# Kernel optimization log

Measured on AMD Instinct MI355X. Metric: run time of the kernel, lower is better.

Reference implementation:

```python
import jax, jax.numpy as jnp
import numpy as np

BIG = 1e9            # stand-in for np.inf so arithmetic stays NaN-free
GRID = 128
BATCH = 4
N_SRC = 4
N_RCV = 16
NUM_SWEEPS = 512     # Jacobi sweeps; >= longest causal wavefront path on the grid
MAX_TRACE_STEPS = 512


def setup_inputs() -> dict:
    key = jax.random.key(0)
    k1, k2, k3 = jax.random.split(key, 3)
    # strictly positive speed of sound in [0.5, 1.5] (solver skips s <= 0)
    sos = jax.random.uniform(k1, (BATCH, 1, GRID, GRID), jnp.float32, 0.5, 1.5)
    sources = jax.random.randint(k2, (N_SRC, 2), 0, GRID)
    receivers = jax.random.randint(k3, (N_RCV, 2), 0, GRID)
    return {"sos": sos, "sources": sources, "receivers": receivers}


def _eikonal_solve(T, dt):
    """Jacobi fixed-point iteration of the heap-based FMM upwind update.
    T: [B,S,N,N] arrival times (BIG == +inf), dt: [B,1,N,N] slowness (1/speed)."""
    def step(T, _):
        pad = [(0, 0)] * (T.ndim - 2) + [(1, 1), (1, 1)]
        Tp = jnp.pad(T, pad, constant_values=BIG)
        tx = jnp.minimum(Tp[..., :-2, 1:-1], Tp[..., 2:, 1:-1])   # min x-neighbor
        ty = jnp.minimum(Tp[..., 1:-1, :-2], Tp[..., 1:-1, 2:])   # min y-neighbor
        fx = tx < BIG
        fy = ty < BIG
        txs = jnp.where(fx, tx, 0.0)
        tys = jnp.where(fy, ty, 0.0)
        # quadratic 2 t^2 - 2(tx+ty) t + tx^2 + ty^2 - dt^2 = 0
        # => t = ((tx+ty) + sqrt(2 dt^2 - (tx-ty)^2)) / 2 ; inf if discriminant < 0
        disc = 2.0 * dt * dt - (txs - tys) ** 2
        sq = jnp.where(disc > 0, jnp.sqrt(jnp.maximum(disc, 1e-30)), 0.0)
        quad = jnp.where(disc >= 0, 0.5 * (txs + tys + sq), BIG)
        tent = jnp.where(fx & fy, quad,
                         jnp.where(fx, txs + dt, jnp.where(fy, tys + dt, BIG)))
        return jnp.minimum(T, tent), None
    T, _ = jax.lax.scan(step, T, None, length=NUM_SWEEPS)
    return T


def _backtrace(T, sources, receivers):
    """Steepest-descent walk from each receiver to its emitter, summing T along
    the path (mirrors update_tof_matrix)."""
    B, S, nx, ny = T.shape
    R = receivers.shape[0]
    ei = jnp.broadcast_to(sources[:, 0][None, :, None], (B, S, R))
    ej = jnp.broadcast_to(sources[:, 1][None, :, None], (B, S, R))
    i0 = jnp.broadcast_to(receivers[:, 0][None, None, :], (B, S, R))
    j0 = jnp.broadcast_to(receivers[:, 1][None, None, :], (B, S, R))
    bI = jnp.arange(B)[None, :, None, None]
    sI = jnp.arange(S)[None, None, :, None]

    def step(state, _):
        i, j, t, done = state
        ci = jnp.stack([i - 1, i + 1, i, i], 0)        # [4,B,S,R]
        cj = jnp.stack([j, j, j - 1, j + 1], 0)
        valid = (ci >= 0) & (ci < nx) & (cj >= 0) & (cj < ny)
        tv = T[bI, sI, jnp.clip(ci, 0, nx - 1), jnp.clip(cj, 0, ny - 1)]
        tv = jnp.where(valid, tv, BIG)
        k = jnp.argmin(tv, axis=0)[None]               # [1,B,S,R]
        ni = jnp.take_along_axis(ci, k, 0)[0]
        nj = jnp.take_along_axis(cj, k, 0)[0]
        tn = jnp.take_along_axis(tv, k, 0)[0]
        i2 = jnp.where(done, i, ni)
        j2 = jnp.where(done, j, nj)
        t2 = t + jnp.where(done, 0.0, tn)
        done2 = done | ((i2 == ei) & (j2 == ej))
        return (i2, j2, t2, done2), None

    done0 = (i0 == ei) & (j0 == ej)
    t0 = jnp.zeros((B, S, R), T.dtype)
    (_, _, t, _), _ = jax.lax.scan(step, (i0, j0, t0, done0), None,
                                   length=MAX_TRACE_STEPS)
    return t


def reference(sos, sources, receivers):
    B, _, nx, ny = sos.shape
    S = sources.shape[0]
    R = receivers.shape[0]
    speed = sos[:, 0]                                              # [B,N,N]
    dt = jnp.where(speed > 0, 1.0 / jnp.maximum(speed, 1e-12), BIG)[:, None]
    T0 = jnp.full((B, S, nx, ny), BIG, sos.dtype)
    T0 = T0.at[:, jnp.arange(S), sources[:, 0], sources[:, 1]].set(0.0)
    T = _eikonal_solve(T0, dt)
    times = _backtrace(T, sources, receivers)                       # [B,S,R]
    tof = jnp.full((B, nx, ny), jnp.inf, sos.dtype)
    return tof.at[:, :S, :R].set(times)
```

## Files before the change

### kernel.cpp

```cpp
#include <hip/hip_runtime.h>
#include <math.h>

#define BIGF 1000000000.0f
#define GRIDN 128
#define STRT 130
#define LSZ 16960
#define NTRACE 512
#define MAXCYC 96

template<bool LEAN>
__device__ __forceinline__ float cellUpd(float tx, float ty, float dtv, float cur) {
    if (LEAN) {
        float A2  = 2.0f * dtv * dtv;
        float diff = tx - ty;
        float disc = __builtin_fmaf(-diff, diff, A2);
        float sq   = __builtin_amdgcn_sqrtf(disc);
        float quad = 0.5f * ((tx + ty) + sq);
        float tent = (disc >= 0.0f) ? quad : BIGF;
        return fminf(cur, tent);
    } else {
        bool fx = tx < BIGF;
        bool fy = ty < BIGF;
        float txs = fx ? tx : 0.0f;
        float tys = fy ? ty : 0.0f;
        float A2  = 2.0f * dtv * dtv;
        float diff = txs - tys;
        float disc = __builtin_fmaf(-diff, diff, A2);
        float sq   = __builtin_amdgcn_sqrtf(disc);
        float sum1 = txs + tys;
        float quad = (disc >= 0.0f) ? 0.5f * (sum1 + sq) : BIGF;
        float tent = (fx && fy) ? quad : ((fx || fy) ? (sum1 + dtv) : BIGF);
        return fminf(cur, tent);
    }
}

__device__ __forceinline__ void ldsMin(float* p, float v) {
    atomicMin((unsigned int*)p, __float_as_uint(v));
}

template<int CTRL>
__device__ __forceinline__ float dppf(float oldv, float src) {
    return __int_as_float(__builtin_amdgcn_update_dpp(
        __float_as_int(oldv), __float_as_int(src), CTRL, 0xF, 0xF, false));
}

template<int SI, int SJ, bool LEAN>
__device__ int sweepDiag(float* __restrict__ Tl, const float* __restrict__ dtl,
                         int l, int dp0) {
    const int pr0 = (SI > 0) ? l : 127 - l;
    const int pr1 = (SI > 0) ? l + 64 : 63 - l;
    const int rb0 = (pr0 + 1) * STRT + ((SJ > 0) ? 0 : 127);
    const int rb1 = (pr1 + 1) * STRT + ((SJ > 0) ? 0 : 127);
#define ADR0(c) ((SJ > 0) ? rb0 + (c) : rb0 - (c))
#define ADR1(c) ((SJ > 0) ? rb1 + (c) : rb1 - (c))
    int c0 = (dp0 - l) & 127;
    int c1 = c0 ^ 64;
    float prev0 = Tl[ADR0(c0) - SJ];
    float prev1 = Tl[ADR1(c1) - SJ];
    float cur0  = Tl[ADR0(c0)],              cur1  = Tl[ADR1(c1)];
    float rt0   = Tl[ADR0((c0 + 1) & 127)],  rt1   = Tl[ADR1((c1 + 1) & 127)];
    float rtA0  = Tl[ADR0((c0 + 2) & 127)],  rtA1  = Tl[ADR1((c1 + 2) & 127)];
    float dt0   = dtl[ADR0(c0)],             dt1   = dtl[ADR1(c1)];
    float dtA0  = dtl[ADR0((c0 + 1) & 127)], dtA1  = dtl[ADR1((c1 + 1) & 127)];
    bool changed = false;
    bool sawBig  = false;
#pragma unroll 4
    for (int step = 0; step < 128; ++step) {
        float up0 = dppf<0x138>(BIGF, prev0);
        float t_r = dppf<0x13C>(0.0f, prev0);
        float up1 = dppf<0x138>(t_r, prev1);
        float t_l = dppf<0x134>(0.0f, rt1);
        float dn0 = dppf<0x130>(t_l, rt0);
        float dn1 = dppf<0x130>(BIGF, rt1);
        float pl0 = (c0 == 0)   ? BIGF : prev0;
        float pl1 = (c0 == 64)  ? BIGF : prev1;
        float rr0 = (c0 == 127) ? BIGF : rt0;
        float rr1 = (c0 == 63)  ? BIGF : rt1;
        float n0 = cellUpd<LEAN>(fminf(up0, dn0), fminf(pl0, rr0), dt0, cur0);
        float n1 = cellUpd<LEAN>(fminf(up1, dn1), fminf(pl1, rr1), dt1, cur1);
        changed |= (n0 < cur0) | (n1 < cur1);
        if (!LEAN) sawBig |= (n0 == BIGF) | (n1 == BIGF);
        ldsMin(&Tl[ADR0(c0)], n0);
        ldsMin(&Tl[ADR1(c1)], n1);
        int p0 = (c0 + 3) & 127;
        int q0 = (c0 + 2) & 127;
        float rtB0 = Tl[ADR0(p0)];
        float rtB1 = Tl[ADR1(p0 ^ 64)];
        float dtB0 = dtl[ADR0(q0)];
        float dtB1 = dtl[ADR1(q0 ^ 64)];
        prev0 = n0;  prev1 = n1;
        cur0 = rt0;  cur1 = rt1;
        rt0 = rtA0;  rt1 = rtA1;  rtA0 = rtB0;  rtA1 = rtB1;
        dt0 = dtA0;  dt1 = dtA1;  dtA0 = dtB0;  dtA1 = dtB1;
        c0 = (c0 + 1) & 127;
        c1 = c0 ^ 64;
    }
#undef ADR0
#undef ADR1
    int r = __any((int)changed) ? 1 : 0;
    if (!LEAN && __any((int)sawBig)) r |= 2;
    return r;
}

template<bool LEAN>
__device__ __forceinline__ int dispatchSweep(float* Tl, const float* dtl,
                                             int dir, int l, int lag) {
    if      (dir == 0) return sweepDiag<+1, +1, LEAN>(Tl, dtl, l, lag);
    else if (dir == 1) return sweepDiag<-1, -1, LEAN>(Tl, dtl, l, lag);
    else if (dir == 2) return sweepDiag<+1, -1, LEAN>(Tl, dtl, l, lag);
    else               return sweepDiag<-1, +1, LEAN>(Tl, dtl, l, lag);
}

__global__ __launch_bounds__(768) void eik_solve(
    const float* __restrict__ sos, const int* __restrict__ src,
    const int* __restrict__ rcv, float* __restrict__ out)
{
    __shared__ __align__(16) float Tl[LSZ];
    __shared__ __align__(16) float dtl[LSZ];
    __shared__ int flags[13];

    const int tid = threadIdx.x;
    const int w   = tid >> 6;
    const int dir = w & 3;
    const int lag = (w >> 2) * 85;
    const int l   = tid & 63;
    const int bs  = blockIdx.x;
    const int b   = bs >> 2;
    const int s   = bs & 3;

    for (int idx = tid * 4; idx < LSZ; idx += 768 * 4) {
        *(float4*)&Tl[idx]  = make_float4(BIGF, BIGF, BIGF, BIGF);
        *(float4*)&dtl[idx] = make_float4(BIGF, BIGF, BIGF, BIGF);
    }
    __syncthreads();

    const float* sg = sos + b * (GRIDN * GRIDN);
    for (int q = tid; q < GRIDN * 64; q += 768) {
        int r = q >> 6, c2 = (q & 63) << 1;
        float2 sp = *(const float2*)&sg[r * GRIDN + c2];
        float2 dv;
        dv.x = (sp.x > 0.0f) ? 1.0f / fmaxf(sp.x, 1e-12f) : BIGF;
        dv.y = (sp.y > 0.0f) ? 1.0f / fmaxf(sp.y, 1e-12f) : BIGF;
        *(float2*)&dtl[(r + 1) * STRT + c2] = dv;
    }
    const int si = src[2 * s], sj = src[2 * s + 1];
    __syncthreads();
    if (tid == 0) Tl[(si + 1) * STRT + sj] = 0.0f;

    bool lean = false;
    for (int cyc = 0; cyc < MAXCYC; ++cyc) {
        if (tid < 13) flags[tid] = 0;
        __syncthreads();
        int r = lean ? dispatchSweep<true>(Tl, dtl, dir, l, lag)
                     : dispatchSweep<false>(Tl, dtl, dir, l, lag);
        if (l == 0) {
            if (r & 1) flags[w] = 1;
            if (r & 2) flags[12] = 1;
        }
        __syncthreads();
        int any = flags[0] | flags[1] | flags[2]  | flags[3]
                | flags[4] | flags[5] | flags[6]  | flags[7]
                | flags[8] | flags[9] | flags[10] | flags[11];
        int big = flags[12];
        __syncthreads();
        if (!any) break;
        if (!lean && !big) lean = true;
    }

    if (tid < 16) {
        int i = rcv[2 * tid + 0];
        int j = rcv[2 * tid + 1];
        bool done = (i == si) && (j == sj);
        float t = 0.0f;
        for (int st = 0; st < NTRACE; ++st) {
            if (__all((int)done)) break;
            int p = (i + 1) * STRT + j;
            float t0v = Tl[p - STRT];
            float t1v = Tl[p + STRT];
            float t2v = Tl[p - 1];
            float t3v = Tl[p + 1];
            float best = t0v; int kb = 0;
            if (t1v < best) { best = t1v; kb = 1; }
            if (t2v < best) { best = t2v; kb = 2; }
            if (t3v < best) { best = t3v; kb = 3; }
            int ni = i + ((kb == 0) ? -1 : (kb == 1) ? 1 : 0);
            int nj = j + ((kb == 2) ? -1 : (kb == 3) ? 1 : 0);
            if (!done) { i = ni; j = nj; t += best; }
            done = done || ((i == si) && (j == sj));
        }
        out[b * GRIDN * GRIDN + s * GRIDN + tid] = t;
    }
}

__global__ void fill_big(float* __restrict__ out) {
    int idx = blockIdx.x * 256 + threadIdx.x;
    out[idx] = BIGF;
}

extern "C" void kernel_launch(void* const* d_in, const int* in_sizes, int n_in,
                              void* d_out, int out_size, void* d_ws, size_t ws_size,
                              hipStream_t stream) {
    const float* sos = (const float*)d_in[0];
    const int*   src = (const int*)d_in[1];
    const int*   rcv = (const int*)d_in[2];
    float* out = (float*)d_out;

    hipLaunchKernelGGL(fill_big, dim3(256), dim3(256), 0, stream, out);
    hipLaunchKernelGGL(eik_solve, dim3(16), dim3(768), 0, stream, sos, src, rcv, out);
}
```

Baseline: 287.5 us.

## Interleave three diagonal sweep phases per wave and cut block to four waves

Each wave now carries three independent diagonal wavefronts (phases 0, 42 and 85) in registers, work that three separate waves used to do. The block drops from 768 to 256 threads and the convergence flags shrink to match. The aim is more instruction-level parallelism inside a wave, hiding the DPP, LDS and sqrt latency of the dependent chain, with fewer waves contending for LDS atomics. The cost is much higher register pressure and fewer waves per CU to hide latency, and the interleaving changes the order of updates within a sweep, which may change how many cycles are needed to converge.

```diff
diff --git a/kernel.cpp b/kernel.cpp
--- a/kernel.cpp
+++ b/kernel.cpp
@@ -45,55 +45,70 @@
 }
 
 template<int SI, int SJ, bool LEAN>
-__device__ int sweepDiag(float* __restrict__ Tl, const float* __restrict__ dtl,
-                         int l, int dp0) {
+__device__ int sweepDiag3(float* __restrict__ Tl, const float* __restrict__ dtl,
+                          int l) {
     const int pr0 = (SI > 0) ? l : 127 - l;
     const int pr1 = (SI > 0) ? l + 64 : 63 - l;
     const int rb0 = (pr0 + 1) * STRT + ((SJ > 0) ? 0 : 127);
     const int rb1 = (pr1 + 1) * STRT + ((SJ > 0) ? 0 : 127);
 #define ADR0(c) ((SJ > 0) ? rb0 + (c) : rb0 - (c))
 #define ADR1(c) ((SJ > 0) ? rb1 + (c) : rb1 - (c))
-    int c0 = (dp0 - l) & 127;
-    int c1 = c0 ^ 64;
-    float prev0 = Tl[ADR0(c0) - SJ];
-    float prev1 = Tl[ADR1(c1) - SJ];
-    float cur0  = Tl[ADR0(c0)],              cur1  = Tl[ADR1(c1)];
-    float rt0   = Tl[ADR0((c0 + 1) & 127)],  rt1   = Tl[ADR1((c1 + 1) & 127)];
-    float rtA0  = Tl[ADR0((c0 + 2) & 127)],  rtA1  = Tl[ADR1((c1 + 2) & 127)];
-    float dt0   = dtl[ADR0(c0)],             dt1   = dtl[ADR1(c1)];
-    float dtA0  = dtl[ADR0((c0 + 1) & 127)], dtA1  = dtl[ADR1((c1 + 1) & 127)];
+    int   c0[3];
+    float prev0[3], prev1[3], cur0[3], cur1[3], rt0[3], rt1[3];
+    float rtA0[3], rtA1[3], dt0v[3], dt1v[3], dtA0[3], dtA1[3];
+    const int PH0 = 0, PH1 = 42, PH2 = 85;
     bool changed = false;
     bool sawBig  = false;
-#pragma unroll 4
+#pragma unroll
+    for (int k = 0; k < 3; ++k) {
+        int ph = (k == 0) ? PH0 : (k == 1) ? PH1 : PH2;
+        int cc = (ph - l) & 127;
+        int c1 = cc ^ 64;
+        c0[k] = cc;
+        prev0[k] = Tl[ADR0(cc) - SJ];
+        prev1[k] = Tl[ADR1(c1) - SJ];
+        cur0[k]  = Tl[ADR0(cc)];              cur1[k]  = Tl[ADR1(c1)];
+        rt0[k]   = Tl[ADR0((cc + 1) & 127)];  rt1[k]   = Tl[ADR1((c1 + 1) & 127)];
+        rtA0[k]  = Tl[ADR0((cc + 2) & 127)];  rtA1[k]  = Tl[ADR1((c1 + 2) & 127)];
+        dt0v[k]  = dtl[ADR0(cc)];             dt1v[k]  = dtl[ADR1(c1)];
+        dtA0[k]  = dtl[ADR0((cc + 1) & 127)]; dtA1[k]  = dtl[ADR1((c1 + 1) & 127)];
+    }
+#pragma unroll 2
     for (int step = 0; step < 128; ++step) {
-        float up0 = dppf<0x138>(BIGF, prev0);
-        float t_r = dppf<0x13C>(0.0f, prev0);
-        float up1 = dppf<0x138>(t_r, prev1);
-        float t_l = dppf<0x134>(0.0f, rt1);
-        float dn0 = dppf<0x130>(t_l, rt0);
-        float dn1 = dppf<0x130>(BIGF, rt1);
-        float pl0 = (c0 == 0)   ? BIGF : prev0;
-        float pl1 = (c0 == 64)  ? BIGF : prev1;
-        float rr0 = (c0 == 127) ? BIGF : rt0;
-        float rr1 = (c0 == 63)  ? BIGF : rt1;
-        float n0 = cellUpd<LEAN>(fminf(up0, dn0), fminf(pl0, rr0), dt0, cur0);
-        float n1 = cellUpd<LEAN>(fminf(up1, dn1), fminf(pl1, rr1), dt1, cur1);
-        changed |= (n0 < cur0) | (n1 < cur1);
-        if (!LEAN) sawBig |= (n0 == BIGF) | (n1 == BIGF);
-        ldsMin(&Tl[ADR0(c0)], n0);
-        ldsMin(&Tl[ADR1(c1)], n1);
-        int p0 = (c0 + 3) & 127;
-        int q0 = (c0 + 2) & 127;
-        float rtB0 = Tl[ADR0(p0)];
-        float rtB1 = Tl[ADR1(p0 ^ 64)];
-        float dtB0 = dtl[ADR0(q0)];
-        float dtB1 = dtl[ADR1(q0 ^ 64)];
-        prev0 = n0;  prev1 = n1;
-        cur0 = rt0;  cur1 = rt1;
-        rt0 = rtA0;  rt1 = rtA1;  rtA0 = rtB0;  rtA1 = rtB1;
-        dt0 = dtA0;  dt1 = dtA1;  dtA0 = dtB0;  dtA1 = dtB1;
-        c0 = (c0 + 1) & 127;
-        c1 = c0 ^ 64;
+#pragma unroll
+        for (int k = 0; k < 3; ++k) {
+            int cc = c0[k];
+            int c1 = cc ^ 64;
+            float up0 = dppf<0x138>(BIGF, prev0[k]);
+            float t_r = dppf<0x13C>(0.0f, prev0[k]);
+            float up1 = dppf<0x138>(t_r, prev1[k]);
+            float t_l = dppf<0x134>(0.0f, rt1[k]);
+            float dn0 = dppf<0x130>(t_l, rt0[k]);
+            float dn1 = dppf<0x130>(BIGF, rt1[k]);
+            float pl0 = (cc == 0)   ? BIGF : prev0[k];
+            float pl1 = (cc == 64)  ? BIGF : prev1[k];
+            float rr0 = (cc == 127) ? BIGF : rt0[k];
+            float rr1 = (cc == 63)  ? BIGF : rt1[k];
+            float n0 = cellUpd<LEAN>(fminf(up0, dn0), fminf(pl0, rr0), dt0v[k], cur0[k]);
+            float n1 = cellUpd<LEAN>(fminf(up1, dn1), fminf(pl1, rr1), dt1v[k], cur1[k]);
+            changed |= (n0 < cur0[k]) | (n1 < cur1[k]);
+            if (!LEAN) sawBig |= (n0 == BIGF) | (n1 == BIGF);
+            ldsMin(&Tl[ADR0(cc)], n0);
+            ldsMin(&Tl[ADR1(c1)], n1);
+            int p0 = (cc + 3) & 127;
+            int q0 = (cc + 2) & 127;
+            float rtB0 = Tl[ADR0(p0)];
+            float rtB1 = Tl[ADR1(p0 ^ 64)];
+            float dtB0 = dtl[ADR0(q0)];
+            float dtB1 = dtl[ADR1(q0 ^ 64)];
+            prev0[k] = n0;      prev1[k] = n1;
+            cur0[k] = rt0[k];   cur1[k] = rt1[k];
+            rt0[k] = rtA0[k];   rt1[k] = rtA1[k];
+            rtA0[k] = rtB0;     rtA1[k] = rtB1;
+            dt0v[k] = dtA0[k];  dt1v[k] = dtA1[k];
+            dtA0[k] = dtB0;     dtA1[k] = dtB1;
+            c0[k] = (cc + 1) & 127;
+        }
     }
 #undef ADR0
 #undef ADR1
@@ -104,38 +119,36 @@
 
 template<bool LEAN>
 __device__ __forceinline__ int dispatchSweep(float* Tl, const float* dtl,
-                                             int dir, int l, int lag) {
-    if      (dir == 0) return sweepDiag<+1, +1, LEAN>(Tl, dtl, l, lag);
-    else if (dir == 1) return sweepDiag<-1, -1, LEAN>(Tl, dtl, l, lag);
-    else if (dir == 2) return sweepDiag<+1, -1, LEAN>(Tl, dtl, l, lag);
-    else               return sweepDiag<-1, +1, LEAN>(Tl, dtl, l, lag);
-}
-
-__global__ __launch_bounds__(768) void eik_solve(
+                                             int dir, int l) {
+    if      (dir == 0) return sweepDiag3<+1, +1, LEAN>(Tl, dtl, l);
+    else if (dir == 1) return sweepDiag3<-1, -1, LEAN>(Tl, dtl, l);
+    else if (dir == 2) return sweepDiag3<+1, -1, LEAN>(Tl, dtl, l);
+    else               return sweepDiag3<-1, +1, LEAN>(Tl, dtl, l);
+}
+
+__global__ __launch_bounds__(256) void eik_solve(
     const float* __restrict__ sos, const int* __restrict__ src,
     const int* __restrict__ rcv, float* __restrict__ out)
 {
     __shared__ __align__(16) float Tl[LSZ];
     __shared__ __align__(16) float dtl[LSZ];
-    __shared__ int flags[13];
+    __shared__ int flags[5];
 
     const int tid = threadIdx.x;
     const int w   = tid >> 6;
-    const int dir = w & 3;
-    const int lag = (w >> 2) * 85;
     const int l   = tid & 63;
     const int bs  = blockIdx.x;
     const int b   = bs >> 2;
     const int s   = bs & 3;
 
-    for (int idx = tid * 4; idx < LSZ; idx += 768 * 4) {
+    for (int idx = tid * 4; idx < LSZ; idx += 256 * 4) {
         *(float4*)&Tl[idx]  = make_float4(BIGF, BIGF, BIGF, BIGF);
         *(float4*)&dtl[idx] = make_float4(BIGF, BIGF, BIGF, BIGF);
     }
     __syncthreads();
 
     const float* sg = sos + b * (GRIDN * GRIDN);
-    for (int q = tid; q < GRIDN * 64; q += 768) {
+    for (int q = tid; q < GRIDN * 64; q += 256) {
         int r = q >> 6, c2 = (q & 63) << 1;
         float2 sp = *(const float2*)&sg[r * GRIDN + c2];
         float2 dv;
@@ -149,19 +162,17 @@
 
     bool lean = false;
     for (int cyc = 0; cyc < MAXCYC; ++cyc) {
-        if (tid < 13) flags[tid] = 0;
+        if (tid < 5) flags[tid] = 0;
         __syncthreads();
-        int r = lean ? dispatchSweep<true>(Tl, dtl, dir, l, lag)
-                     : dispatchSweep<false>(Tl, dtl, dir, l, lag);
+        int r = lean ? dispatchSweep<true>(Tl, dtl, w, l)
+                     : dispatchSweep<false>(Tl, dtl, w, l);
         if (l == 0) {
             if (r & 1) flags[w] = 1;
-            if (r & 2) flags[12] = 1;
+            if (r & 2) flags[4] = 1;
         }
         __syncthreads();
-        int any = flags[0] | flags[1] | flags[2]  | flags[3]
-                | flags[4] | flags[5] | flags[6]  | flags[7]
-                | flags[8] | flags[9] | flags[10] | flags[11];
-        int big = flags[12];
+        int any = flags[0] | flags[1] | flags[2] | flags[3];
+        int big = flags[4];
         __syncthreads();
         if (!any) break;
         if (!lean && !big) lean = true;
@@ -206,5 +217,5 @@
     float* out = (float*)d_out;
 
     hipLaunchKernelGGL(fill_big, dim3(256), dim3(256), 0, stream, out);
-    hipLaunchKernelGGL(eik_solve, dim3(16), dim3(768), 0, stream, sos, src, rcv, out);
-}
+    hipLaunchKernelGGL(eik_solve, dim3(16), dim3(256), 0, stream, sos, src, rcv, out);
+}
```

After: 511.2 us. +77.8%, slower.
